# Kernel tuning notes

Hardware: AMD Instinct MI355X
Metric: run time of the kernel (lower is better)

The kernel has to match this reference:

```python
import jax, jax.numpy as jnp
import numpy as np

B, T, D, H, HS = 4, 1024, 1024, 16, 64
DW, DA, DG, DV = 64, 64, 128, 32
DM = H * HS  # == D here
EPS = 1e-5
DECAY_C = -0.606531  # -exp(-0.5)


def setup_inputs() -> dict:
    key = jax.random.key(0)
    ks = jax.random.split(key, 24)
    n = lambda k, s: jax.random.normal(k, s, dtype=jnp.float32)
    w = lambda k, s: n(k, s) * (1.0 / np.sqrt(s[0]))
    return dict(
        current=n(ks[0], (B, T, D)),
        prev=n(ks[1], (B, T, D)),
        v_first=n(ks[2], (B, T, DM)),
        rwkvag=jax.random.uniform(ks[3], (6, D), dtype=jnp.float32),
        rw_W=w(ks[4], (D, D)),
        w1=w(ks[5], (D, DW)), w2=w(ks[6], (DW, DM)), w2_b=n(ks[7], (DM,)) * 0.1,
        kw_W=w(ks[8], (D, DM)), vw_W=w(ks[9], (D, DM)),
        a1=w(ks[10], (D, DA)), a2=w(ks[11], (DA, DM)), a2_b=n(ks[12], (DM,)) * 0.1,
        v1=w(ks[13], (D, DV)), v2=w(ks[14], (DV, DM)), v2_b=n(ks[15], (DM,)) * 0.1,
        g1=w(ks[16], (D, DG)), g2=w(ks[17], (DG, DM)), g2_b=n(ks[18], (DM,)) * 0.1,
        k_k=jnp.ones((DM,)), k_a=jax.random.uniform(ks[19], (DM,), dtype=jnp.float32),
        r_k=jnp.ones((DM,)),
        gn_scale=jnp.ones((DM,)), gn_bias=jnp.zeros((DM,)),
        out_W=w(ks[20], (DM, D)),
    )


def _add_heads(x):
    return x.reshape(x.shape[:-1] + (H, HS))


def reference(current, prev, v_first, rwkvag, rw_W, w1, w2, w2_b, kw_W, vw_W,
              a1, a2, a2_b, v1, v2, v2_b, g1, g2, g2_b,
              k_k, k_a, r_k, gn_scale, gn_bias, out_W):
    diff = prev - current
    # per-channel token-shift mixing for the 6 branches: (B,T,6,D)
    x6 = current[..., None, :] + rwkvag * diff[..., None, :]
    xr, xw, xk, xv, xa, xg = (x6[..., i, :] for i in range(6))

    r = xr @ rw_W
    wl = jnp.tanh(xw @ w1) @ w2 + w2_b          # w-LoRA (tanh, bias_post)
    k = xk @ kw_W
    v = xv @ vw_W
    a = jax.nn.sigmoid((xa @ a1) @ a2 + a2_b)   # a-LoRA (bias_post) + sigmoid
    g = jax.nn.sigmoid(xg @ g1) @ g2 + g2_b     # g-LoRA (sigmoid act)

    kk = _add_heads(k * k_k)
    kk = kk / jnp.linalg.norm(kk, axis=-1, keepdims=True)
    k = k * (1.0 + (a - 1.0) * k_a)
    v = v + (v_first - v) * jax.nn.sigmoid((xv @ v1) @ v2 + v2_b)
    wdec = jnp.exp(DECAY_C * jax.nn.sigmoid(wl))  # decay in (exp(-0.6065), 1)

    rk_sum = _add_heads(r * k * r_k).sum(-1, keepdims=True)  # (B,T,H,1)
    rh, wh, kh, vh = _add_heads(r), _add_heads(wdec), _add_heads(k), _add_heads(v)
    at = -kk
    bt = kk * _add_heads(a)

    def step(state, xs):
        rt, wt, ktt, vt, att, btt = xs  # each (B,H,HS)
        sa = jnp.einsum('bhvk,bhk->bhv', state, att)
        state = (state * wt[:, :, None, :]
                 + sa[..., None] * btt[:, :, None, :]
                 + vt[..., None] * ktt[:, :, None, :])
        y = jnp.einsum('bhvk,bhk->bhv', state, rt)
        return state, y

    xs = tuple(jnp.moveaxis(x, 1, 0) for x in (rh, wh, kh, vh, at, bt))
    state0 = jnp.zeros((B, H, HS, HS), dtype=current.dtype)
    state, ys = jax.lax.scan(step, state0, xs)
    out = jnp.moveaxis(ys, 0, 1)  # (B,T,H,HS)

    # GroupNorm with n_head groups (normalize within each head)
    mu = out.mean(-1, keepdims=True)
    var = out.var(-1, keepdims=True)
    outn = (out - mu) * jax.lax.rsqrt(var + EPS)
    outn = outn.reshape(B, T, DM) * gn_scale + gn_bias

    outn = outn + (rk_sum * vh).reshape(B, T, DM)
    y = (outn * g) @ out_W
    return y, state, v_first
```

## Files before the change

kernel.cpp:

```cpp
#include <hip/hip_runtime.h>
#include <math.h>

#define NT 4096
#define DD 1024
#define NH 16
#define HSZ 64
#define GN_EPS 1e-5f
#define DECAY_C -0.606531f

typedef __attribute__((ext_vector_type(8))) short short8;
typedef __attribute__((ext_vector_type(4))) float float4v;

#define GLB(p) ((const __attribute__((address_space(1))) void*)(p))
#define LDS(p) ((__attribute__((address_space(3))) void*)(p))

__device__ __forceinline__ float sigm(float x) { return 1.f / (1.f + __expf(-x)); }

__device__ __forceinline__ unsigned short f2bf(float f) {
    unsigned int u = __float_as_uint(f);
    u = (u + 0x7fffu + ((u >> 16) & 1u)) >> 16;
    return (unsigned short)u;
}
__device__ __forceinline__ float bf2f(unsigned short h) {
    return __uint_as_float(((unsigned int)h) << 16);
}

__device__ __forceinline__ float row_sum16(float x) {
    int t;
    t = __builtin_amdgcn_update_dpp(0, __float_as_int(x), 0x128, 0xF, 0xF, true);
    x += __int_as_float(t);
    t = __builtin_amdgcn_update_dpp(0, __float_as_int(x), 0x124, 0xF, 0xF, true);
    x += __int_as_float(t);
    t = __builtin_amdgcn_update_dpp(0, __float_as_int(x), 0x122, 0xF, 0xF, true);
    x += __int_as_float(t);
    t = __builtin_amdgcn_update_dpp(0, __float_as_int(x), 0x121, 0xF, 0xF, true);
    x += __int_as_float(t);
    return x;
}

__global__ __launch_bounds__(256)
void mix6(const float* __restrict__ cur, const float* __restrict__ prev,
          const float* __restrict__ lam,
          ushort* __restrict__ xrh, ushort* __restrict__ xrl,
          ushort* __restrict__ xwh, ushort* __restrict__ xwl,
          ushort* __restrict__ xkh, ushort* __restrict__ xkl,
          ushort* __restrict__ xvh, ushort* __restrict__ xvl,
          ushort* __restrict__ xah, ushort* __restrict__ xal,
          ushort* __restrict__ xgh, ushort* __restrict__ xgl)
{
    const int tok = blockIdx.x;
    const int d0 = threadIdx.x * 4;
    const size_t base = (size_t)tok * DD + d0;
    float4 c = *(const float4*)(cur + base);
    float4 p = *(const float4*)(prev + base);
    float dx = p.x - c.x, dy = p.y - c.y, dz = p.z - c.z, dw = p.w - c.w;
    ushort* hs[6] = {xrh, xwh, xkh, xvh, xah, xgh};
    ushort* ls[6] = {xrl, xwl, xkl, xvl, xal, xgl};
#pragma unroll
    for (int j = 0; j < 6; j++) {
        float4 l = *(const float4*)(lam + j * DD + d0);
        float m0 = c.x + l.x * dx;
        float m1 = c.y + l.y * dy;
        float m2 = c.z + l.z * dz;
        float m3 = c.w + l.w * dw;
        ushort4 h;
        h.x = f2bf(m0); h.y = f2bf(m1); h.z = f2bf(m2); h.w = f2bf(m3);
        *(ushort4*)(hs[j] + base) = h;
        ushort4 lo;
        lo.x = f2bf(m0 - bf2f(h.x));
        lo.y = f2bf(m1 - bf2f(h.y));
        lo.z = f2bf(m2 - bf2f(h.z));
        lo.w = f2bf(m3 - bf2f(h.w));
        *(ushort4*)(ls[j] + base) = lo;
    }
}

__global__ __launch_bounds__(256)
void transpose_pad(const float* __restrict__ W, ushort* __restrict__ Wh,
                   ushort* __restrict__ Wl, int K, int N)
{
    __shared__ float tile[32][33];
    const int bx = blockIdx.x * 32;
    const int by = blockIdx.y * 32;
    const int tx = threadIdx.x, ty = threadIdx.y;
#pragma unroll
    for (int i = 0; i < 32; i += 8) {
        float v = 0.f;
        if (bx + tx < N) v = W[(size_t)(by + ty + i) * N + bx + tx];
        tile[ty + i][tx] = v;
    }
    __syncthreads();
#pragma unroll
    for (int i = 0; i < 32; i += 8) {
        float v = tile[tx][ty + i];
        ushort h = f2bf(v);
        size_t o = (size_t)(bx + ty + i) * K + by + tx;
        Wh[o] = h;
        if (Wl) Wl[o] = f2bf(v - bf2f(h));
    }
}

#define SWZ(r) (((r) >> 1) & 3)

__global__ __launch_bounds__(256)
void gemm_mega1(const ushort* __restrict__ xrh, const ushort* __restrict__ xrl,
                const ushort* __restrict__ xwh, const ushort* __restrict__ xwl,
                const ushort* __restrict__ xkh, const ushort* __restrict__ xkl,
                const ushort* __restrict__ xvh, const ushort* __restrict__ xvl,
                const ushort* __restrict__ xah, const ushort* __restrict__ xal,
                const ushort* __restrict__ xgh, const ushort* __restrict__ xgl,
                const ushort* __restrict__ Bth, const ushort* __restrict__ Btl,
                float* __restrict__ r_buf, float* __restrict__ k_buf,
                float* __restrict__ v_buf,
                ushort* __restrict__ hwh, ushort* __restrict__ hwl,
                ushort* __restrict__ hah, ushort* __restrict__ hal,
                ushort* __restrict__ hvh, ushort* __restrict__ hvl,
                ushort* __restrict__ hgh, ushort* __restrict__ hgl)
{
    __shared__ ushort As[2][2][128 * 32];
    __shared__ ushort Bs[2][2][128 * 32];
    const int cb = blockIdx.y;
    const ushort* Ah; const ushort* Al;
    if (cb < 8)       { Ah = xrh; Al = xrl; }
    else if (cb < 16) { Ah = xkh; Al = xkl; }
    else if (cb < 24) { Ah = xvh; Al = xvl; }
    else if (cb == 24){ Ah = xwh; Al = xwl; }
    else if (cb == 25){ Ah = xah; Al = xal; }
    else if (cb == 26){ Ah = xvh; Al = xvl; }
    else              { Ah = xgh; Al = xgl; }

    const int tid = threadIdx.x;
    const int rowBase = blockIdx.x * 128;
    const int colBase = cb * 128;
    const int lane = tid & 63;
    const int wave = tid >> 6;
    const int wm = wave >> 1, wn = wave & 1;
    const int m15 = lane & 15, quad = lane >> 4;

    float4v zero4 = {0.f, 0.f, 0.f, 0.f};
    float4v acc[4][4];
#pragma unroll
    for (int i = 0; i < 4; i++)
#pragma unroll
        for (int j = 0; j < 4; j++) acc[i][j] = zero4;

#define STAGE1(kk, bb) do {                                                       \
    const int k0_ = (kk) * 32;                                                    \
    _Pragma("unroll")                                                             \
    for (int i_ = 0; i_ < 2; i_++) {                                              \
        int idx_ = i_ * 256 + tid;                                                \
        int r_ = idx_ >> 2, seg_ = idx_ & 3;                                      \
        int sg_ = seg_ ^ SWZ(r_);       \
        size_t aoff_ = (size_t)(rowBase + r_) * 1024 + k0_ + sg_ * 8;             \
        size_t boff_ = (size_t)(colBase + r_) * 1024 + k0_ + sg_ * 8;             \
        int dst_ = (i_ * 256 + (tid & ~63)) * 8;                                  \
        __builtin_amdgcn_global_load_lds(GLB(Ah + aoff_),  LDS(&As[bb][0][0] + dst_), 16, 0, 0); \
        __builtin_amdgcn_global_load_lds(GLB(Al + aoff_),  LDS(&As[bb][1][0] + dst_), 16, 0, 0); \
        __builtin_amdgcn_global_load_lds(GLB(Bth + boff_), LDS(&Bs[bb][0][0] + dst_), 16, 0, 0); \
        __builtin_amdgcn_global_load_lds(GLB(Btl + boff_), LDS(&Bs[bb][1][0] + dst_), 16, 0, 0); \
    }                                                                             \
} while (0)

    STAGE1(0, 0);
    __syncthreads();

    for (int kt = 0; kt < 32; kt++) {
        const int buf = kt & 1;
        if (kt < 31) STAGE1(kt + 1, buf ^ 1);

        short8 ah[4], bh[4], al[4], bl[4];
#pragma unroll
        for (int mi = 0; mi < 4; mi++) {
            int ra = wm * 64 + mi * 16 + m15;
            int cs = (quad ^ SWZ(ra)) * 8;
            ah[mi] = *(const short8*)(&As[buf][0][0] + ra * 32 + cs);
            al[mi] = *(const short8*)(&As[buf][1][0] + ra * 32 + cs);
        }
#pragma unroll
        for (int ni = 0; ni < 4; ni++) {
            int rb = wn * 64 + ni * 16 + m15;
            int cs = (quad ^ SWZ(rb)) * 8;
            bh[ni] = *(const short8*)(&Bs[buf][0][0] + rb * 32 + cs);
            bl[ni] = *(const short8*)(&Bs[buf][1][0] + rb * 32 + cs);
        }
#pragma unroll
        for (int mi = 0; mi < 4; mi++)
#pragma unroll
            for (int ni = 0; ni < 4; ni++) {
                acc[mi][ni] = __builtin_amdgcn_mfma_f32_16x16x32_bf16(al[mi], bh[ni], acc[mi][ni], 0, 0, 0);
                acc[mi][ni] = __builtin_amdgcn_mfma_f32_16x16x32_bf16(ah[mi], bl[ni], acc[mi][ni], 0, 0, 0);
                acc[mi][ni] = __builtin_amdgcn_mfma_f32_16x16x32_bf16(ah[mi], bh[ni], acc[mi][ni], 0, 0, 0);
            }
        __syncthreads();
    }
#undef STAGE1

#pragma unroll
    for (int mi = 0; mi < 4; mi++) {
#pragma unroll
        for (int ni = 0; ni < 4; ni++) {
            int c = wn * 64 + ni * 16 + m15;
#pragma unroll
            for (int rr = 0; rr < 4; rr++) {
                int row = rowBase + wm * 64 + mi * 16 + quad * 4 + rr;
                float v = acc[mi][ni][rr];
                if (cb < 24) {
                    float* dst = (cb < 8) ? r_buf : (cb < 16) ? k_buf : v_buf;
                    int n = (cb & 7) * 128 + c;
                    dst[(size_t)row * 1024 + n] = v;
                } else if (cb == 24) {
                    if (c < 64) {
                        float t = tanhf(v);
                        ushort h = f2bf(t);
                        hwh[(size_t)row * 64 + c] = h;
                        hwl[(size_t)row * 64 + c] = f2bf(t - bf2f(h));
                    }
                } else if (cb == 25) {
                    if (c < 64) {
                        ushort h = f2bf(v);
                        hah[(size_t)row * 64 + c] = h;
                        hal[(size_t)row * 64 + c] = f2bf(v - bf2f(h));
                    }
                } else if (cb == 26) {
                    if (c < 32) {
                        ushort h = f2bf(v);
                        hvh[(size_t)row * 32 + c] = h;
                        hvl[(size_t)row * 32 + c] = f2bf(v - bf2f(h));
                    }
                } else {
                    float t = sigm(v);
                    ushort h = f2bf(t);
                    hgh[(size_t)row * 128 + c] = h;
                    hgl[(size_t)row * 128 + c] = f2bf(t - bf2f(h));
                }
            }
        }
    }
}

__global__ __launch_bounds__(256)
void gemm_mega2(const ushort* __restrict__ hwh, const ushort* __restrict__ hwl,
                const ushort* __restrict__ hah, const ushort* __restrict__ hal,
                const ushort* __restrict__ hvh, const ushort* __restrict__ hvl,
                const ushort* __restrict__ hgh, const ushort* __restrict__ hgl,
                const ushort* __restrict__ w2Th, const ushort* __restrict__ w2Tl,
                const ushort* __restrict__ a2Th, const ushort* __restrict__ a2Tl,
                const ushort* __restrict__ v2Th, const ushort* __restrict__ v2Tl,
                const ushort* __restrict__ g2Th, const ushort* __restrict__ g2Tl,
                const float* __restrict__ w2_b, const float* __restrict__ a2_b,
                const float* __restrict__ v2_b, const float* __restrict__ g2_b,
                float* __restrict__ w_buf, float* __restrict__ a_buf,
                float* __restrict__ vg_buf, float* __restrict__ g_buf)
{
    __shared__ ushort AsH[128 * 32];
    __shared__ ushort BsH[128 * 32];
    __shared__ ushort AsL[128 * 32];
    __shared__ ushort BsL[128 * 32];
    const int cb = blockIdx.y;
    const int seg = cb >> 3;
    const int K = (seg == 2) ? 32 : (seg == 3) ? 128 : 64;
    const ushort *Ah, *Al, *Bh, *Bl;
    const float* bias;
    float* outp;
    if (seg == 0) { Ah = hwh; Al = hwl; Bh = w2Th; Bl = w2Tl; bias = w2_b; outp = w_buf; }
    else if (seg == 1) { Ah = hah; Al = hal; Bh = a2Th; Bl = a2Tl; bias = a2_b; outp = a_buf; }
    else if (seg == 2) { Ah = hvh; Al = hvl; Bh = v2Th; Bl = v2Tl; bias = v2_b; outp = vg_buf; }
    else { Ah = hgh; Al = hgl; Bh = g2Th; Bl = g2Tl; bias = g2_b; outp = g_buf; }

    const int tid = threadIdx.x;
    const int rowBase = blockIdx.x * 128;
    const int colBase = (cb & 7) * 128;
    const int lane = tid & 63;
    const int wave = tid >> 6;
    const int wm = wave >> 1, wn = wave & 1;
    const int m15 = lane & 15, quad = lane >> 4;

    float4v zero4 = {0.f, 0.f, 0.f, 0.f};
    float4v acc[4][4];
#pragma unroll
    for (int i = 0; i < 4; i++)
#pragma unroll
        for (int j = 0; j < 4; j++) acc[i][j] = zero4;

    for (int k0 = 0; k0 < K; k0 += 32) {
#pragma unroll
        for (int i = 0; i < 2; i++) {
            int idx = i * 256 + tid;
            int r = idx >> 2, s8 = idx & 3;
            int sg = s8 ^ SWZ(r);
            size_t aoff = (size_t)(rowBase + r) * K + k0 + sg * 8;
            size_t boff = (size_t)(colBase + r) * K + k0 + sg * 8;
            int dst = (i * 256 + (tid & ~63)) * 8;
            __builtin_amdgcn_global_load_lds(GLB(Ah + aoff), LDS(AsH + dst), 16, 0, 0);
            __builtin_amdgcn_global_load_lds(GLB(Bh + boff), LDS(BsH + dst), 16, 0, 0);
            __builtin_amdgcn_global_load_lds(GLB(Al + aoff), LDS(AsL + dst), 16, 0, 0);
            __builtin_amdgcn_global_load_lds(GLB(Bl + boff), LDS(BsL + dst), 16, 0, 0);
        }
        __syncthreads();
        short8 ah[4], bh[4], al[4], bl[4];
#pragma unroll
        for (int mi = 0; mi < 4; mi++) {
            int ra = wm * 64 + mi * 16 + m15;
            int cs = (quad ^ SWZ(ra)) * 8;
            ah[mi] = *(const short8*)(AsH + ra * 32 + cs);
            al[mi] = *(const short8*)(AsL + ra * 32 + cs);
        }
#pragma unroll
        for (int ni = 0; ni < 4; ni++) {
            int rb = wn * 64 + ni * 16 + m15;
            int cs = (quad ^ SWZ(rb)) * 8;
            bh[ni] = *(const short8*)(BsH + rb * 32 + cs);
            bl[ni] = *(const short8*)(BsL + rb * 32 + cs);
        }
#pragma unroll
        for (int mi = 0; mi < 4; mi++)
#pragma unroll
            for (int ni = 0; ni < 4; ni++) {
                acc[mi][ni] = __builtin_amdgcn_mfma_f32_16x16x32_bf16(al[mi], bh[ni], acc[mi][ni], 0, 0, 0);
                acc[mi][ni] = __builtin_amdgcn_mfma_f32_16x16x32_bf16(ah[mi], bl[ni], acc[mi][ni], 0, 0, 0);
                acc[mi][ni] = __builtin_amdgcn_mfma_f32_16x16x32_bf16(ah[mi], bh[ni], acc[mi][ni], 0, 0, 0);
            }
        __syncthreads();
    }

#pragma unroll
    for (int mi = 0; mi < 4; mi++) {
#pragma unroll
        for (int ni = 0; ni < 4; ni++) {
            int col = colBase + wn * 64 + ni * 16 + m15;
            float bv = bias[col];
#pragma unroll
            for (int rr = 0; rr < 4; rr++) {
                int row = rowBase + wm * 64 + mi * 16 + quad * 4 + rr;
                float v = acc[mi][ni][rr] + bv;
                if (seg == 1 || seg == 2) v = sigm(v);
                outp[(size_t)row * 1024 + col] = v;
            }
        }
    }
}

__global__ __launch_bounds__(256)
void gemm_bf16s(const ushort* __restrict__ Ah, const ushort* __restrict__ Bh,
                float* __restrict__ outF, int N, int K)
{
    __shared__ ushort As2[2][128 * 32];
    __shared__ ushort Bs2[2][128 * 32];
    const int tid = threadIdx.x;
    const int rowBase = blockIdx.x * 128;
    const int colBase = blockIdx.y * 128;
    const int lane = tid & 63;
    const int wave = tid >> 6;
    const int wm = wave >> 1, wn = wave & 1;
    const int m15 = lane & 15, quad = lane >> 4;

    float4v zero4 = {0.f, 0.f, 0.f, 0.f};
    float4v acc[4][4];
#pragma unroll
    for (int i = 0; i < 4; i++)
#pragma unroll
        for (int j = 0; j < 4; j++) acc[i][j] = zero4;

#define STAGE3(kk, bb) do {                                                       \
    const int k0_ = (kk) * 32;                                                    \
    _Pragma("unroll")                                                             \
    for (int i_ = 0; i_ < 2; i_++) {                                              \
        int idx_ = i_ * 256 + tid;                                                \
        int r_ = idx_ >> 2, seg_ = idx_ & 3;                                      \
        int sg_ = seg_ ^ SWZ(r_);                                                 \
        size_t aoff_ = (size_t)(rowBase + r_) * K + k0_ + sg_ * 8;                \
        size_t boff_ = (size_t)(colBase + r_) * K + k0_ + sg_ * 8;                \
        int dst_ = (i_ * 256 + (tid & ~63)) * 8;                                  \
        __builtin_amdgcn_global_load_lds(GLB(Ah + aoff_), LDS(&As2[bb][0] + dst_), 16, 0, 0); \
        __builtin_amdgcn_global_load_lds(GLB(Bh + boff_), LDS(&Bs2[bb][0] + dst_), 16, 0, 0); \
    }                                                                             \
} while (0)

    const int nk = K >> 5;
    STAGE3(0, 0);
    __syncthreads();

    for (int kt = 0; kt < nk; kt++) {
        const int buf = kt & 1;
        if (kt < nk - 1) STAGE3(kt + 1, buf ^ 1);
        short8 ah[4], bh[4];
#pragma unroll
        for (int mi = 0; mi < 4; mi++) {
            int ra = wm * 64 + mi * 16 + m15;
            ah[mi] = *(const short8*)(&As2[buf][0] + ra * 32 + (quad ^ SWZ(ra)) * 8);
        }
#pragma unroll
        for (int ni = 0; ni < 4; ni++) {
            int rb = wn * 64 + ni * 16 + m15;
            bh[ni] = *(const short8*)(&Bs2[buf][0] + rb * 32 + (quad ^ SWZ(rb)) * 8);
        }
#pragma unroll
        for (int mi = 0; mi < 4; mi++)
#pragma unroll
            for (int ni = 0; ni < 4; ni++)
                acc[mi][ni] = __builtin_amdgcn_mfma_f32_16x16x32_bf16(ah[mi], bh[ni], acc[mi][ni], 0, 0, 0);
        __syncthreads();
    }
#undef STAGE3

#pragma unroll
    for (int mi = 0; mi < 4; mi++) {
#pragma unroll
        for (int ni = 0; ni < 4; ni++) {
            int col = colBase + wn * 64 + ni * 16 + m15;
#pragma unroll
            for (int rr = 0; rr < 4; rr++) {
                int row = rowBase + wm * 64 + mi * 16 + quad * 4 + rr;
                outF[(size_t)row * N + col] = acc[mi][ni][rr];
            }
        }
    }
}

__global__ __launch_bounds__(256)
void elemwise1(const float* __restrict__ r_buf, float* __restrict__ wl_buf,
               float* __restrict__ k_buf, float* __restrict__ v_buf,
               float* __restrict__ kkn_buf, const float* __restrict__ a_buf,
               const float* __restrict__ vg_buf, const float* __restrict__ vfirst,
               const float* __restrict__ kkw, const float* __restrict__ kaw,
               const float* __restrict__ rkw, float* __restrict__ rk_sum)
{
    const int tok = blockIdx.x;
    const int tid = threadIdx.x;
    const int d0 = tid * 4;
    const size_t base = (size_t)tok * DD + d0;

    float4 k0 = *(const float4*)(k_buf + base);
    float4 a4 = *(const float4*)(a_buf + base);
    float4 wl = *(const float4*)(wl_buf + base);
    float4 v0 = *(const float4*)(v_buf + base);
    float4 vg = *(const float4*)(vg_buf + base);
    float4 vf = *(const float4*)(vfirst + base);
    float4 r4 = *(const float4*)(r_buf + base);
    float4 kkc = *(const float4*)(kkw + d0);
    float4 kac = *(const float4*)(kaw + d0);
    float4 rkc = *(const float4*)(rkw + d0);

    float kk0 = k0.x * kkc.x, kk1 = k0.y * kkc.y, kk2 = k0.z * kkc.z, kk3 = k0.w * kkc.w;
    float ss = kk0 * kk0 + kk1 * kk1 + kk2 * kk2 + kk3 * kk3;
    ss += __shfl_xor(ss, 1); ss += __shfl_xor(ss, 2);
    ss += __shfl_xor(ss, 4); ss += __shfl_xor(ss, 8);
    float rn = rsqrtf(ss);
    float4 kkn = { kk0 * rn, kk1 * rn, kk2 * rn, kk3 * rn };
    *(float4*)(kkn_buf + base) = kkn;

    float4 kf;
    kf.x = k0.x * (1.f + (a4.x - 1.f) * kac.x);
    kf.y = k0.y * (1.f + (a4.y - 1.f) * kac.y);
    kf.z = k0.z * (1.f + (a4.z - 1.f) * kac.z);
    kf.w = k0.w * (1.f + (a4.w - 1.f) * kac.w);
    *(float4*)(k_buf + base) = kf;

    float rk = r4.x * kf.x * rkc.x + r4.y * kf.y * rkc.y + r4.z * kf.z * rkc.z + r4.w * kf.w * rkc.w;
    rk += __shfl_xor(rk, 1); rk += __shfl_xor(rk, 2);
    rk += __shfl_xor(rk, 4); rk += __shfl_xor(rk, 8);
    if ((tid & 15) == 0) rk_sum[(size_t)tok * NH + (tid >> 4)] = rk;

    float4 vfin;
    vfin.x = v0.x + (vf.x - v0.x) * vg.x;
    vfin.y = v0.y + (vf.y - v0.y) * vg.y;
    vfin.z = v0.z + (vf.z - v0.z) * vg.z;
    vfin.w = v0.w + (vf.w - v0.w) * vg.w;
    *(float4*)(v_buf + base) = vfin;

    float4 wd;
    wd.x = __expf(DECAY_C * sigm(wl.x));
    wd.y = __expf(DECAY_C * sigm(wl.y));
    wd.z = __expf(DECAY_C * sigm(wl.z));
    wd.w = __expf(DECAY_C * sigm(wl.w));
    *(float4*)(wl_buf + base) = wd;
}

__global__ __launch_bounds__(256)
void scan_kernel(const float* __restrict__ r_buf, const float* __restrict__ w_buf,
                 const float* __restrict__ k_buf, const float* __restrict__ kkn_buf,
                 const float* __restrict__ a_buf, const float* __restrict__ v_buf,
                 float* __restrict__ out_scan, float* __restrict__ state_out)
{
    __shared__ float vecJ[2][5][16][64];
    __shared__ float vbuf2[2][16][16];
    __shared__ float ypart[2][16][16][16];
    const int bh = blockIdx.x;
    const int rg = blockIdx.y;
    const int b = bh >> 4, h = bh & 15;
    const int tid = threadIdx.x;
    const int row = tid >> 4, l16 = tid & 15;
    const int lofs = l16 * 4;
    const int rowbase = rg * 16;
    const size_t tok0 = ((size_t)b * 1024) * DD + h * HSZ;
    float s0 = 0.f, s1 = 0.f, s2 = 0.f, s3 = 0.f;

#define STAGE(cc, bb) do {                                                        \
    const int tt_ = tid >> 4;                                                     \
    const int dd4_ = (tid & 15) * 4;                                              \
    size_t gofs_ = tok0 + (size_t)((cc) * 16 + tt_) * DD + dd4_;                  \
    float* db_ = &vecJ[bb][0][0][0] + ((tid >> 6) << 8);                          \
    __builtin_amdgcn_global_load_lds(GLB(r_buf + gofs_),   LDS(db_),        16, 0, 0); \
    __builtin_amdgcn_global_load_lds(GLB(w_buf + gofs_),   LDS(db_ + 1024), 16, 0, 0); \
    __builtin_amdgcn_global_load_lds(GLB(k_buf + gofs_),   LDS(db_ + 2048), 16, 0, 0); \
    __builtin_amdgcn_global_load_lds(GLB(kkn_buf + gofs_), LDS(db_ + 3072), 16, 0, 0); \
    __builtin_amdgcn_global_load_lds(GLB(a_buf + gofs_),   LDS(db_ + 4096), 16, 0, 0); \
    if (tid < 64) {                                                               \
        size_t vofs_ = tok0 + (size_t)((cc) * 16 + (tid >> 2)) * DD + rowbase + (tid & 3) * 4; \
        __builtin_amdgcn_global_load_lds(GLB(v_buf + vofs_), LDS(&vbuf2[bb][0][0]), 16, 0, 0); \
    }                                                                             \
} while (0)

#define LD_TOK(P, tt) do {                                                        \
    P##r = *(const float4*)(vb + (tt) * 64 + lofs);                               \
    P##w = *(const float4*)(vb + 1024 + (tt) * 64 + lofs);                        \
    P##k = *(const float4*)(vb + 2048 + (tt) * 64 + lofs);                        \
    P##q = *(const float4*)(vb + 3072 + (tt) * 64 + lofs);                        \
    P##a = *(const float4*)(vb + 4096 + (tt) * 64 + lofs);                        \
    P##v = vbp[(tt) * 16 + row];                                                  \
} while (0)

#define STEP(P, tt) do {                                                          \
    float sa_ = P##q.x * s0;                                                      \
    sa_ = fmaf(P##q.y, s1, sa_);                                                  \
    sa_ = fmaf(P##q.z, s2, sa_);                                                  \
    sa_ = fmaf(P##q.w, s3, sa_);                                                  \
    sa_ = row_sum16(sa_);                                                         \
    float n0_ = P##q.x * P##a.x, n1_ = P##q.y * P##a.y;                           \
    float n2_ = P##q.z * P##a.z, n3_ = P##q.w * P##a.w;                           \
    float b0_ = fmaf(s0, P##w.x, P##v * P##k.x);                                  \
    float b1_ = fmaf(s1, P##w.y, P##v * P##k.y);                                  \
    float b2_ = fmaf(s2, P##w.z, P##v * P##k.z);                                  \
    float b3_ = fmaf(s3, P##w.w, P##v * P##k.w);                                  \
    s0 = fmaf(sa_, -n0_, b0_);                                                    \
    s1 = fmaf(sa_, -n1_, b1_);                                                    \
    s2 = fmaf(sa_, -n2_, b2_);                                                    \
    s3 = fmaf(sa_, -n3_, b3_);                                                    \
    float yp_ = P##r.x * s0;                                                      \
    yp_ = fmaf(P##r.y, s1, yp_);                                                  \
    yp_ = fmaf(P##r.z, s2, yp_);                                                  \
    yp_ = fmaf(P##r.w, s3, yp_);                                                  \
    ypart[buf][tt][row][l16] = yp_;                                               \
} while (0)

    STAGE(0, 0);
    __syncthreads();

    for (int c = 0; c < 64; c++) {
        const int buf = c & 1;
        if (c < 63) STAGE(c + 1, buf ^ 1);
        const float* vb  = &vecJ[buf][0][0][0];
        const float* vbp = &vbuf2[buf][0][0];
        float4 Ar, Aw, Ak, Aq, Aa; float Av;
        float4 Br, Bw, Bk, Bq, Ba; float Bv;
        LD_TOK(A, 0);
#pragma unroll
        for (int tp = 0; tp < 8; tp++) {
            LD_TOK(B, 2 * tp + 1);
            STEP(A, 2 * tp);
            if (tp < 7) LD_TOK(A, 2 * tp + 2);
            STEP(B, 2 * tp + 1);
        }
        __syncthreads();
        {
            const int t_ = tid >> 4, r_ = tid & 15;
            const float* yp = &ypart[buf][t_][r_][0];
            float4 y0 = *(const float4*)(yp);
            float4 y1 = *(const float4*)(yp + 4);
            float4 y2 = *(const float4*)(yp + 8);
            float4 y3 = *(const float4*)(yp + 12);
            float ys = ((y0.x + y0.y) + (y0.z + y0.w)) + ((y1.x + y1.y) + (y1.z + y1.w))
                     + ((y2.x + y2.y) + (y2.z + y2.w)) + ((y3.x + y3.y) + (y3.z + y3.w));
            out_scan[tok0 + (size_t)(c * 16 + t_) * DD + rowbase + r_] = ys;
        }
    }

#undef STAGE
#undef LD_TOK
#undef STEP

    float* so = state_out + ((size_t)(b * NH + h) * HSZ + rowbase + row) * HSZ + l16 * 4;
    float4 sv = {s0, s1, s2, s3};
    *(float4*)so = sv;
}

__global__ __launch_bounds__(256)
void elemwise2(const float* __restrict__ out_scan, const float* __restrict__ rk_sum,
               const float* __restrict__ v_buf, const float* __restrict__ g_buf,
               const float* __restrict__ gscale, const float* __restrict__ gbias,
               ushort* __restrict__ z_buf)
{
    const int tok = blockIdx.x;
    const int tid = threadIdx.x;
    const int d0 = tid * 4;
    const size_t base = (size_t)tok * DD + d0;

    float4 o = *(const float4*)(out_scan + base);
    float sm = o.x + o.y + o.z + o.w;
    float ss = o.x * o.x + o.y * o.y + o.z * o.z + o.w * o.w;
    sm += __shfl_xor(sm, 1); sm += __shfl_xor(sm, 2);
    sm += __shfl_xor(sm, 4); sm += __shfl_xor(sm, 8);
    ss += __shfl_xor(ss, 1); ss += __shfl_xor(ss, 2);
    ss += __shfl_xor(ss, 4); ss += __shfl_xor(ss, 8);
    float mu = sm * (1.f / 64.f);
    float var = ss * (1.f / 64.f) - mu * mu;
    float rs = rsqrtf(var + GN_EPS);
    float rk = rk_sum[(size_t)tok * NH + (tid >> 4)];

    float4 v4 = *(const float4*)(v_buf + base);
    float4 g4 = *(const float4*)(g_buf + base);
    float4 gs = *(const float4*)(gscale + d0);
    float4 gb = *(const float4*)(gbias + d0);
    ushort4 z;
    z.x = f2bf(((o.x - mu) * rs * gs.x + gb.x + rk * v4.x) * g4.x);
    z.y = f2bf(((o.y - mu) * rs * gs.y + gb.y + rk * v4.y) * g4.y);
    z.z = f2bf(((o.z - mu) * rs * gs.z + gb.z + rk * v4.z) * g4.z);
    z.w = f2bf(((o.w - mu) * rs * gs.w + gb.w + rk * v4.w) * g4.w);
    *(ushort4*)(z_buf + base) = z;
}

extern "C" void kernel_launch(void* const* d_in, const int* in_sizes, int n_in,
                              void* d_out, int out_size, void* d_ws, size_t ws_size,
                              hipStream_t stream) {
    const float* cur    = (const float*)d_in[0];
    const float* prev   = (const float*)d_in[1];
    const float* vfirst = (const float*)d_in[2];
    const float* rwkvag = (const float*)d_in[3];
    const float* rw_W   = (const float*)d_in[4];
    const float* w1     = (const float*)d_in[5];
    const float* w2     = (const float*)d_in[6];
    const float* w2_b   = (const float*)d_in[7];
    const float* kw_W   = (const float*)d_in[8];
    const float* vw_W   = (const float*)d_in[9];
    const float* a1     = (const float*)d_in[10];
    const float* a2     = (const float*)d_in[11];
    const float* a2_b   = (const float*)d_in[12];
    const float* v1     = (const float*)d_in[13];
    const float* v2     = (const float*)d_in[14];
    const float* v2_b   = (const float*)d_in[15];
    const float* g1     = (const float*)d_in[16];
    const float* g2     = (const float*)d_in[17];
    const float* g2_b   = (const float*)d_in[18];
    const float* k_k    = (const float*)d_in[19];
    const float* k_a    = (const float*)d_in[20];
    const float* r_k    = (const float*)d_in[21];
    const float* gn_s   = (const float*)d_in[22];
    const float* gn_b   = (const float*)d_in[23];
    const float* out_W  = (const float*)d_in[24];

    float* out = (float*)d_out;
    float* y_out = out;
    float* state_out = out + (size_t)NT * DD;
    float* vf_out = state_out + (size_t)4 * NH * HSZ * HSZ;

    float* p = (float*)d_ws;
    const size_t big = (size_t)NT * DD;
    const size_t half = big / 2;
    float* r_buf = p;   p += big;
    float* k_buf = p;   p += big;
    float* v_buf = p;   p += big;
    float* xreg = p;
    ushort* xrh = (ushort*)(xreg);            ushort* xrl = (ushort*)(xreg + half);
    ushort* xwh = (ushort*)(xreg + 2*half);   ushort* xwl = (ushort*)(xreg + 3*half);
    ushort* xkh = (ushort*)(xreg + 4*half);   ushort* xkl = (ushort*)(xreg + 5*half);
    ushort* xvh = (ushort*)(xreg + 6*half);   ushort* xvl = (ushort*)(xreg + 7*half);
    ushort* xah = (ushort*)(xreg + 8*half);   ushort* xal = (ushort*)(xreg + 9*half);
    ushort* xgh = (ushort*)(xreg + 10*half);  ushort* xgl = (ushort*)(xreg + 11*half);
    p += 12 * half;
    float* w_buf   = xreg + 0 * half;
    float* a_buf   = xreg + 2 * half;
    float* vg_buf  = xreg + 4 * half;
    float* os_buf  = vg_buf;
    float* g_buf   = xreg + 6 * half;
    float* kkn_buf = xreg + 8 * half;
    float* btreg = p;
    ushort* Bth = (ushort*)btreg;
    ushort* Btl = (ushort*)(btreg + 1835008);
    p += 2 * 1835008;
    ushort* z_bf  = (ushort*)btreg;
    ushort* outTh = (ushort*)(btreg + 2097152);
    ushort* w2Th = (ushort*)p; p += 32768; ushort* w2Tl = (ushort*)p; p += 32768;
    ushort* a2Th = (ushort*)p; p += 32768; ushort* a2Tl = (ushort*)p; p += 32768;
    ushort* v2Th = (ushort*)p; p += 16384; ushort* v2Tl = (ushort*)p; p += 16384;
    ushort* g2Th = (ushort*)p; p += 65536; ushort* g2Tl = (ushort*)p; p += 65536;
    ushort* hwh = (ushort*)p; p += 131072; ushort* hwl = (ushort*)p; p += 131072;
    ushort* hah = (ushort*)p; p += 131072; ushort* hal = (ushort*)p; p += 131072;
    ushort* hvh = (ushort*)p; p += 65536;  ushort* hvl = (ushort*)p; p += 65536;
    ushort* hgh = (ushort*)p; p += 262144; ushort* hgl = (ushort*)p; p += 262144;
    float* rks_buf = p;        p += 65536;

    dim3 blk(256);
    dim3 t32x8(32, 8);

    transpose_pad<<<dim3(32, 32), t32x8, 0, stream>>>(rw_W, Bth + (size_t)0 * 1024,    Btl + (size_t)0 * 1024,    1024, 1024);
    transpose_pad<<<dim3(32, 32), t32x8, 0, stream>>>(kw_W, Bth + (size_t)1024 * 1024, Btl + (size_t)1024 * 1024, 1024, 1024);
    transpose_pad<<<dim3(32, 32), t32x8, 0, stream>>>(vw_W, Bth + (size_t)2048 * 1024, Btl + (size_t)2048 * 1024, 1024, 1024);
    transpose_pad<<<dim3(4, 32), t32x8, 0, stream>>>(w1, Bth + (size_t)3072 * 1024, Btl + (size_t)3072 * 1024, 1024, 64);
    transpose_pad<<<dim3(4, 32), t32x8, 0, stream>>>(a1, Bth + (size_t)3200 * 1024, Btl + (size_t)3200 * 1024, 1024, 64);
    transpose_pad<<<dim3(4, 32), t32x8, 0, stream>>>(v1, Bth + (size_t)3328 * 1024, Btl + (size_t)3328 * 1024, 1024, 32);
    transpose_pad<<<dim3(4, 32), t32x8, 0, stream>>>(g1, Bth + (size_t)3456 * 1024, Btl + (size_t)3456 * 1024, 1024, 128);
    transpose_pad<<<dim3(32, 2), t32x8, 0, stream>>>(w2, w2Th, w2Tl, 64, 1024);
    transpose_pad<<<dim3(32, 2), t32x8, 0, stream>>>(a2, a2Th, a2Tl, 64, 1024);
    transpose_pad<<<dim3(32, 1), t32x8, 0, stream>>>(v2, v2Th, v2Tl, 32, 1024);
    transpose_pad<<<dim3(32, 4), t32x8, 0, stream>>>(g2, g2Th, g2Tl, 128, 1024);

    mix6<<<NT, blk, 0, stream>>>(cur, prev, rwkvag,
                                 xrh, xrl, xwh, xwl, xkh, xkl,
                                 xvh, xvl, xah, xal, xgh, xgl);

    gemm_mega1<<<dim3(32, 28), blk, 0, stream>>>(
        xrh, xrl, xwh, xwl, xkh, xkl, xvh, xvl, xah, xal, xgh, xgl,
        Bth, Btl, r_buf, k_buf, v_buf,
        hwh, hwl, hah, hal, hvh, hvl, hgh, hgl);

    transpose_pad<<<dim3(32, 32), t32x8, 0, stream>>>(out_W, outTh, nullptr, 1024, 1024);

    gemm_mega2<<<dim3(32, 32), blk, 0, stream>>>(
        hwh, hwl, hah, hal, hvh, hvl, hgh, hgl,
        w2Th, w2Tl, a2Th, a2Tl, v2Th, v2Tl, g2Th, g2Tl,
        w2_b, a2_b, v2_b, g2_b,
        w_buf, a_buf, vg_buf, g_buf);

    elemwise1<<<NT, blk, 0, stream>>>(r_buf, w_buf, k_buf, v_buf, kkn_buf, a_buf,
                                      vg_buf, vfirst, k_k, k_a, r_k, rks_buf);

    scan_kernel<<<dim3(64, 4), blk, 0, stream>>>(r_buf, w_buf, k_buf, kkn_buf, a_buf, v_buf,
                                                 os_buf, state_out);

    elemwise2<<<NT, blk, 0, stream>>>(os_buf, rks_buf, v_buf, g_buf, gn_s, gn_b, z_bf);

    gemm_bf16s<<<dim3(32, 8), blk, 0, stream>>>(z_bf, outTh, y_out, 1024, 1024);

    hipMemcpyAsync(vf_out, vfirst, (size_t)NT * DD * sizeof(float),
                   hipMemcpyDeviceToDevice, stream);
}
```

Measured before the change: 543.0 us.

## Deepen GEMM prefetch with manual waitcnt barriers and widen scan token pipelining

The GEMM main loop now prefetches two stages ahead, using explicit s_waitcnt vmcnt counts and raw s_barrier instead of __syncthreads, so the direct-to-LDS global loads for stage k+2 overlap compute on stage k. The scan kernel software-pipelines four token register sets instead of two, which hides LDS load latency in the serial recurrence. It also sets launch_bounds(256,1) on the scan kernel to allow more registers per thread. The cost is higher register pressure and barrier/waitcnt logic that is fragile and depends on the exact count of outstanding loads.

```diff
diff --git a/kernel.cpp b/kernel.cpp
--- a/kernel.cpp
+++ b/kernel.cpp
@@ -13,6 +13,8 @@
 
 #define GLB(p) ((const __attribute__((address_space(1))) void*)(p))
 #define LDS(p) ((__attribute__((address_space(3))) void*)(p))
+
+#define MEMFENCE asm volatile("" ::: "memory")
 
 __device__ __forceinline__ float sigm(float x) { return 1.f / (1.f + __expf(-x)); }
 
@@ -162,11 +164,13 @@
 } while (0)
 
     STAGE1(0, 0);
-    __syncthreads();
+    STAGE1(1, 1);
+    asm volatile("s_waitcnt vmcnt(8)" ::: "memory");
+    __builtin_amdgcn_s_barrier();
+    MEMFENCE;
 
     for (int kt = 0; kt < 32; kt++) {
         const int buf = kt & 1;
-        if (kt < 31) STAGE1(kt + 1, buf ^ 1);
 
         short8 ah[4], bh[4], al[4], bl[4];
 #pragma unroll
@@ -191,7 +195,20 @@
                 acc[mi][ni] = __builtin_amdgcn_mfma_f32_16x16x32_bf16(ah[mi], bl[ni], acc[mi][ni], 0, 0, 0);
                 acc[mi][ni] = __builtin_amdgcn_mfma_f32_16x16x32_bf16(ah[mi], bh[ni], acc[mi][ni], 0, 0, 0);
             }
-        __syncthreads();
+
+        if (kt == 31) break;
+
+        MEMFENCE;
+        __builtin_amdgcn_s_barrier();
+        MEMFENCE;
+        if (kt < 30) {
+            STAGE1(kt + 2, buf);
+            asm volatile("s_waitcnt vmcnt(8)" ::: "memory");
+        } else {
+            asm volatile("s_waitcnt vmcnt(0)" ::: "memory");
+        }
+        __builtin_amdgcn_s_barrier();
+        MEMFENCE;
     }
 #undef STAGE1
 
@@ -476,7 +493,7 @@
     *(float4*)(wl_buf + base) = wd;
 }
 
-__global__ __launch_bounds__(256)
+__global__ __launch_bounds__(256, 1)
 void scan_kernel(const float* __restrict__ r_buf, const float* __restrict__ w_buf,
                  const float* __restrict__ k_buf, const float* __restrict__ kkn_buf,
                  const float* __restrict__ a_buf, const float* __restrict__ v_buf,
@@ -553,13 +570,19 @@
         const float* vbp = &vbuf2[buf][0][0];
         float4 Ar, Aw, Ak, Aq, Aa; float Av;
         float4 Br, Bw, Bk, Bq, Ba; float Bv;
-        LD_TOK(A, 0);
-#pragma unroll
-        for (int tp = 0; tp < 8; tp++) {
-            LD_TOK(B, 2 * tp + 1);
-            STEP(A, 2 * tp);
-            if (tp < 7) LD_TOK(A, 2 * tp + 2);
-            STEP(B, 2 * tp + 1);
+        float4 Cr, Cw, Ck, Cq, Ca; float Cv;
+        float4 Dr, Dw, Dk, Dq, Da; float Dv;
+        LD_TOK(A, 0); LD_TOK(B, 1); LD_TOK(C, 2);
+#pragma unroll
+        for (int i4 = 0; i4 < 4; i4++) {
+            LD_TOK(D, 4 * i4 + 3);
+            STEP(A, 4 * i4);
+            if (4 * i4 + 4 < 16) LD_TOK(A, 4 * i4 + 4);
+            STEP(B, 4 * i4 + 1);
+            if (4 * i4 + 5 < 16) LD_TOK(B, 4 * i4 + 5);
+            STEP(C, 4 * i4 + 2);
+            if (4 * i4 + 6 < 16) LD_TOK(C, 4 * i4 + 6);
+            STEP(D, 4 * i4 + 3);
         }
         __syncthreads();
         {
```

Result: faster. 516.8 us (-4.8%).
